# Optimization experiments

Hardware: AMD Instinct MI355X
Metric: run time of the kernel (lower is better)

Reference implementation:

```python
import jax, jax.numpy as jnp
import numpy as np

HIDDEN = 1024
NUM_HEADS = 16
HEAD_DIM = 64
B, S = 2, 2048


def setup_inputs() -> dict:
    key = jax.random.key(0)
    k1, k2, k3 = jax.random.split(key, 3)
    x = jax.random.normal(k1, (B, S, HIDDEN), dtype=jnp.float32)
    # xavier-uniform style scaling for the projection weights
    lim_qkv = (6.0 / (HIDDEN + 3 * NUM_HEADS * HEAD_DIM)) ** 0.5
    lim_o = (6.0 / (NUM_HEADS * HEAD_DIM + HIDDEN)) ** 0.5
    w_qkv = jax.random.uniform(k2, (HIDDEN, 3 * NUM_HEADS * HEAD_DIM), jnp.float32, -lim_qkv, lim_qkv)
    w_o = jax.random.uniform(k3, (NUM_HEADS * HEAD_DIM, HIDDEN), jnp.float32, -lim_o, lim_o)
    return {"x": x, "w_qkv": w_qkv, "w_o": w_o}


def reference(x, w_qkv, w_o):
    b, s, _ = x.shape
    qkv = jnp.einsum('bsh,hf->bsf', x, w_qkv)               # [b, s, 3*H*D]
    qkv = qkv.reshape(b, s, 3, NUM_HEADS, HEAD_DIM)
    q = jnp.transpose(qkv[:, :, 0], (0, 2, 1, 3))           # [b, h, s, d]
    k = jnp.transpose(qkv[:, :, 1], (0, 2, 3, 1))           # [b, h, d, s]
    v = jnp.transpose(qkv[:, :, 2], (0, 2, 1, 3))           # [b, h, s, d]
    scores = jnp.einsum('bhqd,bhdk->bhqk', q, k) / jnp.sqrt(jnp.float32(HEAD_DIM))
    scores = jax.nn.softmax(scores, axis=-1)                # [b, h, q, k]
    # NOTE: faithful to source bug: sums over q, output indexed by k
    values = jnp.einsum('bhqk,bhkd->bhkd', scores, v)       # [b, h, s, d]
    values = jnp.transpose(values, (0, 2, 1, 3)).reshape(b, s, NUM_HEADS * HEAD_DIM)
    return jnp.einsum('bsf,fh->bsh', values, w_o)
```

## Files before the change

kernel.cpp:

```cpp
#include <hip/hip_runtime.h>
#include <stdint.h>


#define DEV static __device__ __forceinline__

typedef unsigned short u16;
typedef __attribute__((ext_vector_type(4))) float f32x4;
typedef __attribute__((ext_vector_type(16))) float f32x16;
typedef __bf16 bf16x8 __attribute__((ext_vector_type(8)));
typedef __attribute__((ext_vector_type(8))) unsigned short u16x8;
typedef __attribute__((ext_vector_type(4))) unsigned short u16x4;

#define QSCALE 0.18033688011112042f

DEV u16 f2bf(float f) {
    unsigned u = __builtin_bit_cast(unsigned, f);
    u += 0x7fffu + ((u >> 16) & 1u);
    return (u16)(u >> 16);
}
DEV float bf2f(u16 h) {
    unsigned u = ((unsigned)h) << 16;
    return __builtin_bit_cast(float, u);
}

DEV void async_copy16(const void* g, void* l) {
    __builtin_amdgcn_global_load_lds(
        (__attribute__((address_space(1))) void*)(g),
        (__attribute__((address_space(3))) void*)(l), 16, 0, 0);
}


__global__ __launch_bounds__(256) void cast_f32_bf16(
    const float* __restrict__ src, u16* __restrict__ dst, int n4) {
    int i = blockIdx.x * 256 + threadIdx.x;
    if (i >= n4) return;
    f32x4 v = *(const f32x4*)(src + (size_t)i * 4);
    u16x4 o;
#pragma unroll
    for (int j = 0; j < 4; j++) o[j] = f2bf(v[j]);
    *(u16x4*)(dst + (size_t)i * 4) = o;
}

__global__ __launch_bounds__(256) void transpose_cast(
    const float* __restrict__ src, u16* __restrict__ dst, int rows, int cols) {
    __shared__ float tile[32][33];
    int c0 = blockIdx.x * 32, r0 = blockIdx.y * 32;
    int tx = threadIdx.x, ty = threadIdx.y;
#pragma unroll
    for (int i = 0; i < 4; i++)
        tile[ty + i * 8][tx] = src[(size_t)(r0 + ty + i * 8) * cols + c0 + tx];
    __syncthreads();
#pragma unroll
    for (int i = 0; i < 4; i++)
        dst[(size_t)(c0 + ty + i * 8) * rows + r0 + tx] = f2bf(tile[tx][ty + i * 8]);
}

__global__ __launch_bounds__(256) void gemm_qkv(
    const u16* __restrict__ A, const u16* __restrict__ Bt,
    u16* __restrict__ qb, u16* __restrict__ kb, u16* __restrict__ vb) {
    __shared__ __align__(16) u16 smem[128 * 136];
    u16* As = smem;
    u16* Bs = smem + 4096;
    const int t = threadIdx.x;
    const int wave = t >> 6;
    const int lane = t & 63;
    const int quad = lane >> 4;
    const int l16 = lane & 15;
    const int wr = wave >> 1;
    const int wc = wave & 1;
    const int m0 = blockIdx.y * 128;
    const int n0 = blockIdx.x * 128;

    f32x4 acc[4][4];
#pragma unroll
    for (int i = 0; i < 4; i++)
#pragma unroll
        for (int j = 0; j < 4; j++) acc[i][j] = {0.f, 0.f, 0.f, 0.f};

    for (int kt = 0; kt < 1024; kt += 32) {
#pragma unroll
        for (int i = 0; i < 2; i++) {
            int idx = i * 256 + t;
            int row = idx >> 2, kc = idx & 3;
            async_copy16(A + (size_t)(m0 + row) * 1024 + kt + kc * 8, &As[idx * 8]);
            async_copy16(Bt + (size_t)(n0 + row) * 1024 + kt + kc * 8, &Bs[idx * 8]);
        }
        __syncthreads();
        bf16x8 af[4], bfr[4];
#pragma unroll
        for (int mt = 0; mt < 4; mt++)
            af[mt] = *(const bf16x8*)&As[(wr * 64 + mt * 16 + l16) * 32 + quad * 8];
#pragma unroll
        for (int nt = 0; nt < 4; nt++)
            bfr[nt] = *(const bf16x8*)&Bs[(wc * 64 + nt * 16 + l16) * 32 + quad * 8];
#pragma unroll
        for (int mt = 0; mt < 4; mt++)
#pragma unroll
            for (int nt = 0; nt < 4; nt++)
                acc[mt][nt] = __builtin_amdgcn_mfma_f32_16x16x32_bf16(
                    af[mt], bfr[nt], acc[mt][nt], 0, 0, 0);
        __syncthreads();
    }

    const int tsel = n0 >> 10;
    u16* dst = tsel == 0 ? qb : (tsel == 1 ? kb : vb);
    const float scl = tsel == 0 ? QSCALE : 1.0f;
#pragma unroll
    for (int mt = 0; mt < 4; mt++)
#pragma unroll
        for (int nt = 0; nt < 4; nt++) {
            int nn = wc * 64 + nt * 16 + l16;
#pragma unroll
            for (int r = 0; r < 4; r++) {
                int mm = wr * 64 + mt * 16 + quad * 4 + r;
                smem[mm * 136 + nn] = f2bf(acc[mt][nt][r] * scl);
            }
        }
    __syncthreads();
    const int col0 = (l16) * 8;
    const int rowb = (t >> 4);
    const int h0 = (n0 & 1023) >> 6;
#pragma unroll
    for (int i = 0; i < 8; i++) {
        int row = i * 16 + rowb;
        u16x8 v = *(const u16x8*)&smem[row * 136 + col0];
        int h = h0 + (col0 >> 6), d = col0 & 63;
        int mm = m0 + row;
        int b = mm >> 11, s = mm & 2047;
        *(u16x8*)&dst[((size_t)((b * 16 + h) * 2048 + s)) * 64 + d] = v;
    }
}

__global__ __launch_bounds__(256) void gemm_out(
    const u16* __restrict__ A, const u16* __restrict__ Bt,
    float* __restrict__ out) {
    __shared__ __align__(16) u16 As[64 * 32];
    __shared__ __align__(16) u16 Bs[128 * 32];
    const int m0 = blockIdx.y * 64;
    const int n0 = blockIdx.x * 128;
    const int t = threadIdx.x;
    const int wave = t >> 6, lane = t & 63;
    const int quad = lane >> 4, l16 = lane & 15;
    const int wr = wave >> 1, wc = wave & 1;

    f32x4 acc[2][4];
#pragma unroll
    for (int i = 0; i < 2; i++)
#pragma unroll
        for (int j = 0; j < 4; j++) acc[i][j] = {0.f, 0.f, 0.f, 0.f};

    for (int kt = 0; kt < 1024; kt += 32) {
        async_copy16(A + (size_t)(m0 + (t >> 2)) * 1024 + kt + (t & 3) * 8, &As[t * 8]);
#pragma unroll
        for (int i = 0; i < 2; i++) {
            int idx = i * 256 + t;
            int row = idx >> 2, kc = idx & 3;
            async_copy16(Bt + (size_t)(n0 + row) * 1024 + kt + kc * 8, &Bs[idx * 8]);
        }
        __syncthreads();
        bf16x8 af[2], bfr[4];
#pragma unroll
        for (int mt = 0; mt < 2; mt++)
            af[mt] = *(const bf16x8*)&As[(wr * 32 + mt * 16 + l16) * 32 + quad * 8];
#pragma unroll
        for (int nt = 0; nt < 4; nt++)
            bfr[nt] = *(const bf16x8*)&Bs[(wc * 64 + nt * 16 + l16) * 32 + quad * 8];
#pragma unroll
        for (int mt = 0; mt < 2; mt++)
#pragma unroll
            for (int nt = 0; nt < 4; nt++)
                acc[mt][nt] = __builtin_amdgcn_mfma_f32_16x16x32_bf16(
                    af[mt], bfr[nt], acc[mt][nt], 0, 0, 0);
        __syncthreads();
    }
#pragma unroll
    for (int nt = 0; nt < 4; nt++) {
        int nn = n0 + wc * 64 + nt * 16 + l16;
#pragma unroll
        for (int mt = 0; mt < 2; mt++) {
#pragma unroll
            for (int r = 0; r < 4; r++) {
                int mm = m0 + wr * 32 + mt * 16 + quad * 4 + r;
                out[(size_t)mm * 1024 + nn] = acc[mt][nt][r];
            }
        }
    }
}

__global__ __launch_bounds__(256) void attn_pass1(
    const u16* __restrict__ qb, const u16* __restrict__ kb,
    float* __restrict__ lp) {
    __shared__ __align__(16) u16 Ks0[128 * 32];
    __shared__ __align__(16) u16 Ks1[128 * 32];
    const int t = threadIdx.x;
    const int wave = t >> 6;
    const int lane = t & 63;
    const int l32 = lane & 31, half = lane >> 5;
    const int kchunk = blockIdx.x & 1;
    const int qblk = (blockIdx.x >> 1) & 15;
    const int bh = blockIdx.x >> 5;
    const int q0 = qblk * 128 + wave * 32;

    const u16* Qr = qb + (size_t)(bh * 2048 + q0 + l32) * 64 + half * 8;
    bf16x8 a[4];
#pragma unroll
    for (int f = 0; f < 4; f++) a[f] = *(const bf16x8*)&Qr[f * 16];

    const u16* Kbase = kb + (size_t)(bh * 2048 + kchunk * 1024) * 64;
    const int srow = t >> 2, sc = (t & 3) * 8;

    float lsum[16];
#pragma unroll
    for (int r = 0; r < 16; r++) lsum[r] = 0.f;

    for (int kt = 0; kt < 8; kt++) {
#pragma unroll
        for (int rr = 0; rr < 2; rr++) {
            const u16* src = Kbase + (size_t)(kt * 128 + rr * 64 + srow) * 64 + sc;
            async_copy16(src, &Ks0[rr * 2048 + t * 8]);
            async_copy16(src + 32, &Ks1[rr * 2048 + t * 8]);
        }
        __syncthreads();
#pragma unroll
        for (int sub = 0; sub < 4; sub++) {
            const int row = sub * 32 + l32;
            bf16x8 bfr[4];
            bfr[0] = *(const bf16x8*)&Ks0[row * 32 + half * 8];
            bfr[1] = *(const bf16x8*)&Ks0[row * 32 + 16 + half * 8];
            bfr[2] = *(const bf16x8*)&Ks1[row * 32 + half * 8];
            bfr[3] = *(const bf16x8*)&Ks1[row * 32 + 16 + half * 8];
            f32x16 acc;
#pragma unroll
            for (int r = 0; r < 16; r++) acc[r] = 0.f;
#pragma unroll
            for (int f = 0; f < 4; f++)
                acc = __builtin_amdgcn_mfma_f32_32x32x16_bf16(a[f], bfr[f], acc, 0, 0, 0);
#pragma unroll
            for (int r = 0; r < 16; r++)
                lsum[r] += __builtin_amdgcn_exp2f(acc[r]);
        }
        __syncthreads();
    }
#pragma unroll
    for (int r = 0; r < 16; r++) {
        float v = lsum[r];
        v += __shfl_xor(v, 1);
        v += __shfl_xor(v, 2);
        v += __shfl_xor(v, 4);
        v += __shfl_xor(v, 8);
        v += __shfl_xor(v, 16);
        lsum[r] = v;
    }
    if (l32 == 0) {
        float* dst = lp + kchunk * 65536 + bh * 2048 + q0 + half * 4;
#pragma unroll
        for (int r = 0; r < 16; r++)
            dst[(r & 3) + 8 * (r >> 2)] = lsum[r];
    }
}

__global__ __launch_bounds__(256) void attn_pass2(
    const u16* __restrict__ qb, const u16* __restrict__ kb,
    const float* __restrict__ lp, float* __restrict__ cp) {
    __shared__ __align__(16) u16 Qs0[128 * 32];
    __shared__ __align__(16) u16 Qs1[128 * 32];
    __shared__ __align__(16) float li_lds[1024];
    const int t = threadIdx.x;
    const int wave = t >> 6;
    const int lane = t & 63;
    const int l32 = lane & 31, half = lane >> 5;
    const int qchunk = blockIdx.x & 1;
    const int kblk = (blockIdx.x >> 1) & 15;
    const int bh = blockIdx.x >> 5;
    const int k0 = kblk * 128 + wave * 32;

    {
        const int base = bh * 2048 + qchunk * 1024;
        f32x4 p0 = *(const f32x4*)&lp[base + t * 4];
        f32x4 p1 = *(const f32x4*)&lp[65536 + base + t * 4];
        f32x4 li;
#pragma unroll
        for (int j = 0; j < 4; j++) li[j] = 1.0f / (p0[j] + p1[j]);
        *(f32x4*)&li_lds[t * 4] = li;
    }

    const u16* Kr = kb + (size_t)(bh * 2048 + k0 + l32) * 64 + half * 8;
    bf16x8 b[4];
#pragma unroll
    for (int f = 0; f < 4; f++) b[f] = *(const bf16x8*)&Kr[f * 16];

    const u16* Qbase = qb + (size_t)(bh * 2048 + qchunk * 1024) * 64;
    const int srow = t >> 2, sc = (t & 3) * 8;

    float cs = 0.f;
    __syncthreads();

    for (int qt = 0; qt < 8; qt++) {
#pragma unroll
        for (int rr = 0; rr < 2; rr++) {
            const u16* src = Qbase + (size_t)(qt * 128 + rr * 64 + srow) * 64 + sc;
            async_copy16(src, &Qs0[rr * 2048 + t * 8]);
            async_copy16(src + 32, &Qs1[rr * 2048 + t * 8]);
        }
        __syncthreads();
#pragma unroll
        for (int sub = 0; sub < 4; sub++) {
            const int row = sub * 32 + l32;
            bf16x8 af[4];
            af[0] = *(const bf16x8*)&Qs0[row * 32 + half * 8];
            af[1] = *(const bf16x8*)&Qs0[row * 32 + 16 + half * 8];
            af[2] = *(const bf16x8*)&Qs1[row * 32 + half * 8];
            af[3] = *(const bf16x8*)&Qs1[row * 32 + 16 + half * 8];
            f32x16 acc;
#pragma unroll
            for (int r = 0; r < 16; r++) acc[r] = 0.f;
#pragma unroll
            for (int f = 0; f < 4; f++)
                acc = __builtin_amdgcn_mfma_f32_32x32x16_bf16(af[f], b[f], acc, 0, 0, 0);
            const float* lr = &li_lds[qt * 128 + sub * 32 + half * 4];
            f32x4 li0 = *(const f32x4*)&lr[0];
            f32x4 li1 = *(const f32x4*)&lr[8];
            f32x4 li2 = *(const f32x4*)&lr[16];
            f32x4 li3 = *(const f32x4*)&lr[24];
#pragma unroll
            for (int r = 0; r < 4; r++) cs += __builtin_amdgcn_exp2f(acc[r]) * li0[r];
#pragma unroll
            for (int r = 0; r < 4; r++) cs += __builtin_amdgcn_exp2f(acc[4 + r]) * li1[r];
#pragma unroll
            for (int r = 0; r < 4; r++) cs += __builtin_amdgcn_exp2f(acc[8 + r]) * li2[r];
#pragma unroll
            for (int r = 0; r < 4; r++) cs += __builtin_amdgcn_exp2f(acc[12 + r]) * li3[r];
        }
        __syncthreads();
    }
    cs += __shfl_xor(cs, 32);
    if (lane < 32)
        cp[qchunk * 65536 + bh * 2048 + k0 + lane] = cs;
}

__global__ __launch_bounds__(256) void scale_v(
    const u16* __restrict__ vb, const float* __restrict__ cp,
    u16* __restrict__ valsb) {
    int tid = blockIdx.x * 256 + threadIdx.x;
    int base = tid << 3;
    int bh = base >> 17;
    int rem = base & 131071;
    int s = rem >> 6;
    int d0 = rem & 63;
    int ci = bh * 2048 + s;
    float cs = cp[ci] + cp[65536 + ci];
    u16x8 v = *(const u16x8*)(vb + (size_t)base);
    u16x8 o;
#pragma unroll
    for (int i = 0; i < 8; i++) o[i] = f2bf(bf2f(v[i]) * cs);
    int b = bh >> 4, h = bh & 15;
    *(u16x8*)(valsb + (size_t)((b * 2048 + s) * 1024) + h * 64 + d0) = o;
}


extern "C" void kernel_launch(void* const* d_in, const int* in_sizes, int n_in,
                              void* d_out, int out_size, void* d_ws, size_t ws_size,
                              hipStream_t stream) {
    const float* x    = (const float*)d_in[0];
    const float* wqkv = (const float*)d_in[1];
    const float* wo   = (const float*)d_in[2];
    float* out = (float*)d_out;
    char* ws = (char*)d_ws;

    u16* xb      = (u16*)(ws);
    u16* wqkvT   = (u16*)(ws + 8388608);
    u16* woT     = (u16*)(ws + 14680064);
    u16* qb      = (u16*)(ws + 16777216);
    u16* kb      = (u16*)(ws + 25165824);
    u16* vb      = (u16*)(ws + 33554432);
    u16* valsb   = (u16*)(ws + 42467328);
    float* lp    = (float*)(ws);
    float* cp    = (float*)(ws + 1048576);

    cast_f32_bf16<<<4096, 256, 0, stream>>>(x, xb, 1048576);
    transpose_cast<<<dim3(96, 32), dim3(32, 8), 0, stream>>>(wqkv, wqkvT, 1024, 3072);
    transpose_cast<<<dim3(32, 32), dim3(32, 8), 0, stream>>>(wo, woT, 1024, 1024);
    gemm_qkv<<<dim3(24, 32), 256, 0, stream>>>(xb, wqkvT, qb, kb, vb);
    attn_pass1<<<1024, 256, 0, stream>>>(qb, kb, lp);
    attn_pass2<<<1024, 256, 0, stream>>>(qb, kb, lp, cp);
    scale_v<<<2048, 256, 0, stream>>>(vb, cp, valsb);
    gemm_out<<<dim3(8, 64), 256, 0, stream>>>(valsb, woT, out);
}
```

Measured before the change: 198.6 us.

## Merge prep kernels, fuse V scaling into output GEMM, enlarge attention tiles

```diff
diff --git a/kernel.cpp b/kernel.cpp
--- a/kernel.cpp
+++ b/kernel.cpp
@@ -29,30 +29,40 @@
         (__attribute__((address_space(3))) void*)(l), 16, 0, 0);
 }
 
-
-__global__ __launch_bounds__(256) void cast_f32_bf16(
-    const float* __restrict__ src, u16* __restrict__ dst, int n4) {
-    int i = blockIdx.x * 256 + threadIdx.x;
-    if (i >= n4) return;
-    f32x4 v = *(const f32x4*)(src + (size_t)i * 4);
-    u16x4 o;
-#pragma unroll
-    for (int j = 0; j < 4; j++) o[j] = f2bf(v[j]);
-    *(u16x4*)(dst + (size_t)i * 4) = o;
-}
-
-__global__ __launch_bounds__(256) void transpose_cast(
-    const float* __restrict__ src, u16* __restrict__ dst, int rows, int cols) {
-    __shared__ float tile[32][33];
-    int c0 = blockIdx.x * 32, r0 = blockIdx.y * 32;
-    int tx = threadIdx.x, ty = threadIdx.y;
+DEV void transpose_tile(const float* __restrict__ src, u16* __restrict__ dst,
+                        int rows, int cols, int bx, int by, int t, float* tile) {
+    int c0 = bx * 32, r0 = by * 32;
+    int tx = t & 31, ty = t >> 5;
 #pragma unroll
     for (int i = 0; i < 4; i++)
-        tile[ty + i * 8][tx] = src[(size_t)(r0 + ty + i * 8) * cols + c0 + tx];
+        tile[(ty + i * 8) * 33 + tx] = src[(size_t)(r0 + ty + i * 8) * cols + c0 + tx];
     __syncthreads();
 #pragma unroll
     for (int i = 0; i < 4; i++)
-        dst[(size_t)(c0 + ty + i * 8) * rows + r0 + tx] = f2bf(tile[tx][ty + i * 8]);
+        dst[(size_t)(c0 + ty + i * 8) * rows + r0 + tx] = f2bf(tile[tx * 33 + ty + i * 8]);
+}
+
+__global__ __launch_bounds__(256) void prep(
+    const float* __restrict__ x, const float* __restrict__ wqkv,
+    const float* __restrict__ wo, u16* __restrict__ xb,
+    u16* __restrict__ wqkvT, u16* __restrict__ woT) {
+    __shared__ float tile[32 * 33];
+    const int gid = blockIdx.x;
+    const int t = threadIdx.x;
+    if (gid < 4096) {
+        int i = gid * 256 + t;
+        f32x4 v = *(const f32x4*)(x + (size_t)i * 4);
+        u16x4 o;
+#pragma unroll
+        for (int j = 0; j < 4; j++) o[j] = f2bf(v[j]);
+        *(u16x4*)(xb + (size_t)i * 4) = o;
+    } else if (gid < 7168) {
+        int lid = gid - 4096;
+        transpose_tile(wqkv, wqkvT, 1024, 3072, lid % 96, lid / 96, t, tile);
+    } else {
+        int lid = gid - 7168;
+        transpose_tile(wo, woT, 1024, 1024, lid & 31, lid >> 5, t, tile);
+    }
 }
 
 __global__ __launch_bounds__(256) void gemm_qkv(
@@ -131,67 +141,11 @@
     }
 }
 
-__global__ __launch_bounds__(256) void gemm_out(
-    const u16* __restrict__ A, const u16* __restrict__ Bt,
-    float* __restrict__ out) {
-    __shared__ __align__(16) u16 As[64 * 32];
-    __shared__ __align__(16) u16 Bs[128 * 32];
-    const int m0 = blockIdx.y * 64;
-    const int n0 = blockIdx.x * 128;
-    const int t = threadIdx.x;
-    const int wave = t >> 6, lane = t & 63;
-    const int quad = lane >> 4, l16 = lane & 15;
-    const int wr = wave >> 1, wc = wave & 1;
-
-    f32x4 acc[2][4];
-#pragma unroll
-    for (int i = 0; i < 2; i++)
-#pragma unroll
-        for (int j = 0; j < 4; j++) acc[i][j] = {0.f, 0.f, 0.f, 0.f};
-
-    for (int kt = 0; kt < 1024; kt += 32) {
-        async_copy16(A + (size_t)(m0 + (t >> 2)) * 1024 + kt + (t & 3) * 8, &As[t * 8]);
-#pragma unroll
-        for (int i = 0; i < 2; i++) {
-            int idx = i * 256 + t;
-            int row = idx >> 2, kc = idx & 3;
-            async_copy16(Bt + (size_t)(n0 + row) * 1024 + kt + kc * 8, &Bs[idx * 8]);
-        }
-        __syncthreads();
-        bf16x8 af[2], bfr[4];
-#pragma unroll
-        for (int mt = 0; mt < 2; mt++)
-            af[mt] = *(const bf16x8*)&As[(wr * 32 + mt * 16 + l16) * 32 + quad * 8];
-#pragma unroll
-        for (int nt = 0; nt < 4; nt++)
-            bfr[nt] = *(const bf16x8*)&Bs[(wc * 64 + nt * 16 + l16) * 32 + quad * 8];
-#pragma unroll
-        for (int mt = 0; mt < 2; mt++)
-#pragma unroll
-            for (int nt = 0; nt < 4; nt++)
-                acc[mt][nt] = __builtin_amdgcn_mfma_f32_16x16x32_bf16(
-                    af[mt], bfr[nt], acc[mt][nt], 0, 0, 0);
-        __syncthreads();
-    }
-#pragma unroll
-    for (int nt = 0; nt < 4; nt++) {
-        int nn = n0 + wc * 64 + nt * 16 + l16;
-#pragma unroll
-        for (int mt = 0; mt < 2; mt++) {
-#pragma unroll
-            for (int r = 0; r < 4; r++) {
-                int mm = m0 + wr * 32 + mt * 16 + quad * 4 + r;
-                out[(size_t)mm * 1024 + nn] = acc[mt][nt][r];
-            }
-        }
-    }
-}
-
 __global__ __launch_bounds__(256) void attn_pass1(
     const u16* __restrict__ qb, const u16* __restrict__ kb,
     float* __restrict__ lp) {
-    __shared__ __align__(16) u16 Ks0[128 * 32];
-    __shared__ __align__(16) u16 Ks1[128 * 32];
+    __shared__ __align__(16) u16 Ks0[256 * 32];
+    __shared__ __align__(16) u16 Ks1[256 * 32];
     const int t = threadIdx.x;
     const int wave = t >> 6;
     const int lane = t & 63;
@@ -213,16 +167,16 @@
 #pragma unroll
     for (int r = 0; r < 16; r++) lsum[r] = 0.f;
 
-    for (int kt = 0; kt < 8; kt++) {
-#pragma unroll
-        for (int rr = 0; rr < 2; rr++) {
-            const u16* src = Kbase + (size_t)(kt * 128 + rr * 64 + srow) * 64 + sc;
+    for (int kt = 0; kt < 4; kt++) {
+#pragma unroll
+        for (int rr = 0; rr < 4; rr++) {
+            const u16* src = Kbase + (size_t)(kt * 256 + rr * 64 + srow) * 64 + sc;
             async_copy16(src, &Ks0[rr * 2048 + t * 8]);
             async_copy16(src + 32, &Ks1[rr * 2048 + t * 8]);
         }
         __syncthreads();
 #pragma unroll
-        for (int sub = 0; sub < 4; sub++) {
+        for (int sub = 0; sub < 8; sub++) {
             const int row = sub * 32 + l32;
             bf16x8 bfr[4];
             bfr[0] = *(const bf16x8*)&Ks0[row * 32 + half * 8];
@@ -262,8 +216,8 @@
 __global__ __launch_bounds__(256) void attn_pass2(
     const u16* __restrict__ qb, const u16* __restrict__ kb,
     const float* __restrict__ lp, float* __restrict__ cp) {
-    __shared__ __align__(16) u16 Qs0[128 * 32];
-    __shared__ __align__(16) u16 Qs1[128 * 32];
+    __shared__ __align__(16) u16 Qs0[256 * 32];
+    __shared__ __align__(16) u16 Qs1[256 * 32];
     __shared__ __align__(16) float li_lds[1024];
     const int t = threadIdx.x;
     const int wave = t >> 6;
@@ -295,16 +249,16 @@
     float cs = 0.f;
     __syncthreads();
 
-    for (int qt = 0; qt < 8; qt++) {
-#pragma unroll
-        for (int rr = 0; rr < 2; rr++) {
-            const u16* src = Qbase + (size_t)(qt * 128 + rr * 64 + srow) * 64 + sc;
+    for (int qt = 0; qt < 4; qt++) {
+#pragma unroll
+        for (int rr = 0; rr < 4; rr++) {
+            const u16* src = Qbase + (size_t)(qt * 256 + rr * 64 + srow) * 64 + sc;
             async_copy16(src, &Qs0[rr * 2048 + t * 8]);
             async_copy16(src + 32, &Qs1[rr * 2048 + t * 8]);
         }
         __syncthreads();
 #pragma unroll
-        for (int sub = 0; sub < 4; sub++) {
+        for (int sub = 0; sub < 8; sub++) {
             const int row = sub * 32 + l32;
             bf16x8 af[4];
             af[0] = *(const bf16x8*)&Qs0[row * 32 + half * 8];
@@ -317,7 +271,7 @@
 #pragma unroll
             for (int f = 0; f < 4; f++)
                 acc = __builtin_amdgcn_mfma_f32_32x32x16_bf16(af[f], b[f], acc, 0, 0, 0);
-            const float* lr = &li_lds[qt * 128 + sub * 32 + half * 4];
+            const float* lr = &li_lds[qt * 256 + sub * 32 + half * 4];
             f32x4 li0 = *(const f32x4*)&lr[0];
             f32x4 li1 = *(const f32x4*)&lr[8];
             f32x4 li2 = *(const f32x4*)&lr[16];
@@ -338,23 +292,73 @@
         cp[qchunk * 65536 + bh * 2048 + k0 + lane] = cs;
 }
 
-__global__ __launch_bounds__(256) void scale_v(
+__global__ __launch_bounds__(256) void gemm_out(
     const u16* __restrict__ vb, const float* __restrict__ cp,
-    u16* __restrict__ valsb) {
-    int tid = blockIdx.x * 256 + threadIdx.x;
-    int base = tid << 3;
-    int bh = base >> 17;
-    int rem = base & 131071;
-    int s = rem >> 6;
-    int d0 = rem & 63;
-    int ci = bh * 2048 + s;
-    float cs = cp[ci] + cp[65536 + ci];
-    u16x8 v = *(const u16x8*)(vb + (size_t)base);
-    u16x8 o;
-#pragma unroll
-    for (int i = 0; i < 8; i++) o[i] = f2bf(bf2f(v[i]) * cs);
-    int b = bh >> 4, h = bh & 15;
-    *(u16x8*)(valsb + (size_t)((b * 2048 + s) * 1024) + h * 64 + d0) = o;
+    const u16* __restrict__ Bt, float* __restrict__ out) {
+    __shared__ __align__(16) u16 As[64 * 32];
+    __shared__ __align__(16) u16 Bs[128 * 32];
+    const int m0 = blockIdx.y * 64;
+    const int n0 = blockIdx.x * 128;
+    const int t = threadIdx.x;
+    const int wave = t >> 6, lane = t & 63;
+    const int quad = lane >> 4, l16 = lane & 15;
+    const int wr = wave >> 1, wc = wave & 1;
+
+    const int mm = m0 + (t >> 2);
+    const int b = mm >> 11, s = mm & 2047;
+
+    f32x4 acc[2][4];
+#pragma unroll
+    for (int i = 0; i < 2; i++)
+#pragma unroll
+        for (int j = 0; j < 4; j++) acc[i][j] = {0.f, 0.f, 0.f, 0.f};
+
+    for (int kt = 0; kt < 1024; kt += 32) {
+        {
+            int k0 = kt + (t & 3) * 8;
+            int h = k0 >> 6, d = k0 & 63;
+            int ci = (b * 16 + h) * 2048 + s;
+            float csc = cp[ci] + cp[65536 + ci];
+            u16x8 v = *(const u16x8*)&vb[((size_t)ci) * 64 + d];
+            u16x8 o;
+#pragma unroll
+            for (int j = 0; j < 8; j++) o[j] = f2bf(bf2f(v[j]) * csc);
+            *(u16x8*)&As[t * 8] = o;
+        }
+#pragma unroll
+        for (int i = 0; i < 2; i++) {
+            int idx = i * 256 + t;
+            int row = idx >> 2, kc = idx & 3;
+            async_copy16(Bt + (size_t)(n0 + row) * 1024 + kt + kc * 8, &Bs[idx * 8]);
+        }
+        __syncthreads();
+        bf16x8 af[2], bfr[4];
+#pragma unroll
+        for (int mt = 0; mt < 2; mt++)
+            af[mt] = *(const bf16x8*)&As[(wr * 32 + mt * 16 + l16) * 32 + quad * 8];
+#pragma unroll
+        for (int nt = 0; nt < 4; nt++)
+            bfr[nt] = *(const bf16x8*)&Bs[(wc * 64 + nt * 16 + l16) * 32 + quad * 8];
+#pragma unroll
+        for (int mt = 0; mt < 2; mt++)
+#pragma unroll
+            for (int nt = 0; nt < 4; nt++)
+                acc[mt][nt] = __builtin_amdgcn_mfma_f32_16x16x32_bf16(
+                    af[mt], bfr[nt], acc[mt][nt], 0, 0, 0);
+        __syncthreads();
+    }
+#pragma unroll
+    for (int nt = 0; nt < 4; nt++) {
+        int nn = n0 + wc * 64 + nt * 16 + l16;
+#pragma unroll
+        for (int mt = 0; mt < 2; mt++) {
+#pragma unroll
+            for (int r = 0; r < 4; r++) {
+                int mr = m0 + wr * 32 + mt * 16 + quad * 4 + r;
+                out[(size_t)mr * 1024 + nn] = acc[mt][nt][r];
+            }
+        }
+    }
 }
 
 
@@ -373,16 +377,12 @@
     u16* qb      = (u16*)(ws + 16777216);
     u16* kb      = (u16*)(ws + 25165824);
     u16* vb      = (u16*)(ws + 33554432);
-    u16* valsb   = (u16*)(ws + 42467328);
     float* lp    = (float*)(ws);
     float* cp    = (float*)(ws + 1048576);
 
-    cast_f32_bf16<<<4096, 256, 0, stream>>>(x, xb, 1048576);
-    transpose_cast<<<dim3(96, 32), dim3(32, 8), 0, stream>>>(wqkv, wqkvT, 1024, 3072);
-    transpose_cast<<<dim3(32, 32), dim3(32, 8), 0, stream>>>(wo, woT, 1024, 1024);
+    prep<<<8192, 256, 0, stream>>>(x, wqkv, wo, xb, wqkvT, woT);
     gemm_qkv<<<dim3(24, 32), 256, 0, stream>>>(xb, wqkvT, qb, kb, vb);
     attn_pass1<<<1024, 256, 0, stream>>>(qb, kb, lp);
     attn_pass2<<<1024, 256, 0, stream>>>(qb, kb, lp, cp);
-    scale_v<<<2048, 256, 0, stream>>>(vb, cp, valsb);
-    gemm_out<<<dim3(8, 64), 256, 0, stream>>>(valsb, woT, out);
-}
+    gemm_out<<<dim3(8, 64), 256, 0, stream>>>(vb, cp, woT, out);
+}
```

Result: no change. 200.2 us (+0.8%).
